# Kernel optimization log

Hardware: AMD Instinct MI355X
Metric: run time of the kernel (lower is better)

## Reference

```python
import jax, jax.numpy as jnp
import numpy as np

TEMP = 0.07
HARD_K = 512
EMB_D = 768
PROJ_D = 128
QUEUE = 32768
BATCH = 2048
NUM_CLASSES = 2


def setup_inputs() -> dict:
    key = jax.random.key(0)
    ks = jax.random.split(key, 8)
    embeddings = jax.random.normal(ks[0], (BATCH, EMB_D), dtype=jnp.float32)
    labels = jax.random.randint(ks[1], (BATCH,), 0, NUM_CLASSES)
    # projector params: Linear(D,D) -> ReLU -> Linear(D,128)
    W1 = jax.random.normal(ks[2], (EMB_D, EMB_D), dtype=jnp.float32) * 0.02
    b1 = jnp.zeros((EMB_D,), dtype=jnp.float32)
    W2 = jax.random.normal(ks[3], (EMB_D, PROJ_D), dtype=jnp.float32) * 0.02
    b2 = jnp.zeros((PROJ_D,), dtype=jnp.float32)
    # queue buffers: L2-normalized random embeddings (as in __init__) with valid labels
    qe = jax.random.normal(ks[4], (QUEUE, PROJ_D), dtype=jnp.float32)
    queue_embeddings = qe / jnp.linalg.norm(qe, axis=1, keepdims=True)
    queue_labels = jax.random.randint(ks[5], (QUEUE,), 0, NUM_CLASSES)
    return {
        'embeddings': embeddings, 'labels': labels,
        'W1': W1, 'b1': b1, 'W2': W2, 'b2': b2,
        'queue_embeddings': queue_embeddings, 'queue_labels': queue_labels,
    }


def reference(embeddings, labels, W1, b1, W2, b2, queue_embeddings, queue_labels):
    n = embeddings.shape[0]
    # projector + L2 normalize
    h = jax.nn.relu(embeddings @ W1 + b1)
    z = h @ W2 + b2
    z = z / jnp.linalg.norm(z, axis=1, keepdims=True)  # (N, 128)

    # pairwise in-batch similarities, scaled by temperature
    S = (z @ z.T) / TEMP  # (N, N)
    same = labels[:, None] == labels[None, :]
    eye = jnp.eye(n, dtype=bool)
    pos_mask = same & ~eye           # positives: same label, not self
    neg_mask = ~same                 # in-batch negatives: different label

    # logsumexp over in-batch negatives per anchor (-inf rows -> -inf, handled by logaddexp)
    neg_batch = jnp.where(neg_mask, S, -jnp.inf)
    lse_batch = jax.scipy.special.logsumexp(neg_batch, axis=1)  # (N,)

    # hard negatives from queue: opposite-label, top-K by similarity
    sims_q = z @ queue_embeddings.T  # (N, Q)
    opp = (queue_labels[None, :] != labels[:, None]) & (queue_labels[None, :] >= 0)
    masked_q = jnp.where(opp, sims_q, -jnp.inf)
    topk_vals, _ = jax.lax.top_k(masked_q, HARD_K)  # (N, K); -inf pads drop from logsumexp
    # fallback (no opposite-label entries): first K queue embeddings regardless of label
    fallback = sims_q[:, :HARD_K]
    has_opp = opp.any(axis=1, keepdims=True)
    neg_q = jnp.where(has_opp, topk_vals, fallback) / TEMP
    lse_queue = jax.scipy.special.logsumexp(neg_q, axis=1)  # (N,)

    # all negatives for anchor i: batch negatives ++ queue hard negatives
    lse_neg = jnp.logaddexp(lse_batch, lse_queue)  # (N,)

    # per positive pair (i, j): log_prob = pos_sim - logsumexp([pos_sim, negs])
    log_prob = S - jnp.logaddexp(S, lse_neg[:, None])  # (N, N)
    losses = jnp.where(pos_mask, -log_prob, 0.0)
    count = pos_mask.sum()
    return jnp.where(count > 0, losses.sum() / count.astype(losses.dtype), 0.0)
```

## Files before the change

kernel.cpp:

```cpp
#include <hip/hip_runtime.h>
#include <hip/hip_fp16.h>

#define BATCH_N   2048
#define EMB_D_    768
#define PROJ_D_   128
#define QUEUE_N   32768
#define HARD_K_   512
static constexpr float INV_T  = 1.0f / 0.07f;
static constexpr float WLO    = 0.12f;
static constexpr float S8ENC  = 255.0f / 0.88f;
static constexpr float BINW   = 0.88f / 255.0f;

typedef __attribute__((ext_vector_type(8))) short short8;
typedef __attribute__((ext_vector_type(4))) short short4v;
typedef __attribute__((ext_vector_type(4))) float f32x4;

__device__ __forceinline__ unsigned short f2bf(float f) {
    unsigned u = __float_as_uint(f);
    unsigned r = u + 0x7fffu + ((u >> 16) & 1u);
    return (unsigned short)(r >> 16);
}
__device__ __forceinline__ float bf2f(short s) {
    return __uint_as_float(((unsigned)(unsigned short)s) << 16);
}
__device__ __forceinline__ int opp_of(int mylab, const int* __restrict__ qcnt) {
    const int same = (mylab == 0) ? qcnt[0] : ((mylab == 1) ? qcnt[1] : 0);
    return qcnt[2] - same;
}

__global__ void __launch_bounds__(256) mfma_s_pack(const short* __restrict__ Ab,
                                                   const short* __restrict__ Bb,
                                                   short* __restrict__ C, int N) {
    __shared__ __align__(16) short As[128 * 128];
    __shared__ __align__(16) short Bs[128 * 128];
    const int t = threadIdx.x;
    const int lane = t & 63, wv = t >> 6;
    const int l16 = lane & 15, l4 = lane >> 4;
    const int m0 = blockIdx.y * 128, n0 = blockIdx.x * 128;

    #pragma unroll
    for (int it = 0; it < 8; ++it) {
        const int r = it * 4 + wv, row = r * 4 + l4, cg = l16 ^ (row & 15);
        __builtin_amdgcn_global_load_lds(
            (const __attribute__((address_space(1))) void*)(Ab + (size_t)(m0 + row) * 128 + cg * 8),
            (__attribute__((address_space(3))) void*)(As + r * 512), 16, 0, 0);
    }
    #pragma unroll
    for (int it = 0; it < 8; ++it) {
        const int r = it * 4 + wv, row = r * 4 + l4, cg = l16 ^ (row & 15);
        __builtin_amdgcn_global_load_lds(
            (const __attribute__((address_space(1))) void*)(Bb + (size_t)(n0 + row) * 128 + cg * 8),
            (__attribute__((address_space(3))) void*)(Bs + r * 512), 16, 0, 0);
    }
    __syncthreads();

    const int wm = (wv & 1) * 64, wn = (wv >> 1) * 64;
    f32x4 acc[4][4];
    #pragma unroll
    for (int i = 0; i < 4; ++i)
        #pragma unroll
        for (int j = 0; j < 4; ++j) acc[i][j] = f32x4{0.f, 0.f, 0.f, 0.f};

    #pragma unroll
    for (int ks = 0; ks < 4; ++ks) {
        short8 af[4], bfr[4];
        const int ch = (ks * 4 + l4) ^ l16;
        #pragma unroll
        for (int i = 0; i < 4; ++i) {
            af[i]  = *(const short8*)(As + (wm + i * 16 + l16) * 128 + ch * 8);
            bfr[i] = *(const short8*)(Bs + (wn + i * 16 + l16) * 128 + ch * 8);
        }
        #pragma unroll
        for (int i = 0; i < 4; ++i)
            #pragma unroll
            for (int j = 0; j < 4; ++j)
                acc[i][j] = __builtin_amdgcn_mfma_f32_16x16x32_bf16(af[i], bfr[j], acc[i][j], 0, 0, 0);
    }
    #pragma unroll
    for (int i = 0; i < 4; ++i)
        #pragma unroll
        for (int r = 0; r < 4; ++r) {
            const int m = m0 + wm + i * 16 + l4 * 4 + r;
            union { unsigned short u[4]; uint2 d; } pk;
            #pragma unroll
            for (int j = 0; j < 4; ++j) pk.u[j] = f2bf(acc[i][j][r]);
            *(uint2*)(C + (size_t)m * N + n0 + wn + l16 * 4) = pk.d;
        }
}

__global__ void __launch_bounds__(256) mfma_mask8(const short* __restrict__ Ab,
                                                  const short* __restrict__ Bb,
                                                  unsigned char* __restrict__ codes,
                                                  const int* __restrict__ labA,
                                                  const int* __restrict__ labB) {
    __shared__ __align__(16) short As[128 * 128];
    __shared__ __align__(16) short Bs[128 * 128];
    const int t = threadIdx.x;
    const int lane = t & 63, wv = t >> 6;
    const int l16 = lane & 15, l4 = lane >> 4;
    const int m0 = blockIdx.y * 128;
    const int wm = (wv & 1) * 64, wn = (wv >> 1) * 64;

    #pragma unroll
    for (int it = 0; it < 8; ++it) {
        const int r = it * 4 + wv, row = r * 4 + l4, cg = l16 ^ (row & 15);
        __builtin_amdgcn_global_load_lds(
            (const __attribute__((address_space(1))) void*)(Ab + (size_t)(m0 + row) * 128 + cg * 8),
            (__attribute__((address_space(3))) void*)(As + r * 512), 16, 0, 0);
    }
    {
        const int n0 = (blockIdx.x * 4) * 128;
        #pragma unroll
        for (int it = 0; it < 8; ++it) {
            const int r = it * 4 + wv, row = r * 4 + l4, cg = l16 ^ (row & 15);
            __builtin_amdgcn_global_load_lds(
                (const __attribute__((address_space(1))) void*)(Bb + (size_t)(n0 + row) * 128 + cg * 8),
                (__attribute__((address_space(3))) void*)(Bs + r * 512), 16, 0, 0);
        }
    }

    int la[16];
    #pragma unroll
    for (int i = 0; i < 4; ++i)
        #pragma unroll
        for (int r = 0; r < 4; ++r)
            la[i * 4 + r] = labA[m0 + wm + i * 16 + l4 * 4 + r];
    const float C0 = 1.0f - WLO * S8ENC;
    __syncthreads();

    #pragma unroll
    for (int tt = 0; tt < 4; ++tt) {
        const int n0 = (blockIdx.x * 4 + tt) * 128;

        f32x4 acc[4][4];
        #pragma unroll
        for (int i = 0; i < 4; ++i)
            #pragma unroll
            for (int j = 0; j < 4; ++j) acc[i][j] = f32x4{0.f, 0.f, 0.f, 0.f};

        #pragma unroll
        for (int ks = 0; ks < 4; ++ks) {
            short8 af[4], bfr[4];
            const int ch = (ks * 4 + l4) ^ l16;
            #pragma unroll
            for (int i = 0; i < 4; ++i) {
                af[i]  = *(const short8*)(As + (wm + i * 16 + l16) * 128 + ch * 8);
                bfr[i] = *(const short8*)(Bs + (wn + i * 16 + l16) * 128 + ch * 8);
            }
            #pragma unroll
            for (int i = 0; i < 4; ++i)
                #pragma unroll
                for (int j = 0; j < 4; ++j)
                    acc[i][j] = __builtin_amdgcn_mfma_f32_16x16x32_bf16(af[i], bfr[j], acc[i][j], 0, 0, 0);
        }

        if (tt < 3) {
            __syncthreads();
            const int n1 = (blockIdx.x * 4 + tt + 1) * 128;
            #pragma unroll
            for (int it = 0; it < 8; ++it) {
                const int r = it * 4 + wv, row = r * 4 + l4, cg = l16 ^ (row & 15);
                __builtin_amdgcn_global_load_lds(
                    (const __attribute__((address_space(1))) void*)(Bb + (size_t)(n1 + row) * 128 + cg * 8),
                    (__attribute__((address_space(3))) void*)(Bs + r * 512), 16, 0, 0);
            }
        }

        float a0[4], a1[4];
        #pragma unroll
        for (int j = 0; j < 4; ++j) {
            const int q = labB[n0 + wn + j * 16 + l16];
            a0[j] = (q >= 0 && q != 0) ? C0 : -1e9f;
            a1[j] = (q >= 0 && q != 1) ? C0 : -1e9f;
        }
        #pragma unroll
        for (int i = 0; i < 4; ++i) {
            #pragma unroll
            for (int r = 0; r < 4; ++r) {
                const int m  = m0 + wm + i * 16 + l4 * 4 + r;
                const bool z = (la[i * 4 + r] == 0);
                unsigned pk = 0;
                #pragma unroll
                for (int j = 0; j < 4; ++j) {
                    const float add = z ? a0[j] : a1[j];
                    const float f = fmaf(acc[i][j][r], S8ENC, add);
#if __has_builtin(__builtin_amdgcn_cvt_pk_u8_f32)
                    pk = __builtin_amdgcn_cvt_pk_u8_f32(f, j, pk);
#else
                    const unsigned c = (unsigned)fminf(fmaxf(f, 0.0f), 255.0f);
                    pk |= c << (8 * j);
#endif
                }
                *(unsigned*)(codes + (size_t)m * QUEUE_N + n0 + wn + l16 * 4) = pk;
            }
        }
        if (tt < 3) __syncthreads();
    }
}

__global__ void __launch_bounds__(256) mfma_h64(const short* __restrict__ Ab,
                                                const short* __restrict__ Bb,
                                                const float* __restrict__ bias,
                                                short* __restrict__ C,
                                                int N, int K) {
    __shared__ __align__(16) short As[64 * 128];
    __shared__ __align__(16) short Bs[128 * 128];
    const int t = threadIdx.x;
    const int lane = t & 63, wv = t >> 6;
    const int l16 = lane & 15, l4 = lane >> 4;
    const int m0 = blockIdx.y * 64, n0 = blockIdx.x * 128;
    const int wn = wv * 32;

    f32x4 acc[4][2];
    #pragma unroll
    for (int i = 0; i < 4; ++i)
        #pragma unroll
        for (int j = 0; j < 2; ++j) acc[i][j] = f32x4{0.f, 0.f, 0.f, 0.f};

    for (int kb = 0; kb < K; kb += 128) {
        __syncthreads();
        #pragma unroll
        for (int it = 0; it < 4; ++it) {
            const int r = it * 4 + wv, row = r * 4 + l4, cg = l16 ^ (row & 15);
            __builtin_amdgcn_global_load_lds(
                (const __attribute__((address_space(1))) void*)(Ab + (size_t)(m0 + row) * K + kb + cg * 8),
                (__attribute__((address_space(3))) void*)(As + r * 512), 16, 0, 0);
        }
        #pragma unroll
        for (int it = 0; it < 8; ++it) {
            const int r = it * 4 + wv, row = r * 4 + l4, cg = l16 ^ (row & 15);
            __builtin_amdgcn_global_load_lds(
                (const __attribute__((address_space(1))) void*)(Bb + (size_t)(n0 + row) * K + kb + cg * 8),
                (__attribute__((address_space(3))) void*)(Bs + r * 512), 16, 0, 0);
        }
        __syncthreads();
        #pragma unroll
        for (int ks = 0; ks < 4; ++ks) {
            short8 af[4], bfr[2];
            const int ch = (ks * 4 + l4) ^ l16;
            #pragma unroll
            for (int i = 0; i < 4; ++i)
                af[i] = *(const short8*)(As + (i * 16 + l16) * 128 + ch * 8);
            #pragma unroll
            for (int j = 0; j < 2; ++j)
                bfr[j] = *(const short8*)(Bs + (wn + j * 16 + l16) * 128 + ch * 8);
            #pragma unroll
            for (int i = 0; i < 4; ++i)
                #pragma unroll
                for (int j = 0; j < 2; ++j)
                    acc[i][j] = __builtin_amdgcn_mfma_f32_16x16x32_bf16(af[i], bfr[j], acc[i][j], 0, 0, 0);
        }
    }

    float bsv[2];
    #pragma unroll
    for (int j = 0; j < 2; ++j) bsv[j] = bias[n0 + wn + j * 16 + l16];
    #pragma unroll
    for (int i = 0; i < 4; ++i)
        #pragma unroll
        for (int r = 0; r < 4; ++r) {
            const int m = m0 + i * 16 + l4 * 4 + r;
            #pragma unroll
            for (int j = 0; j < 2; ++j) {
                const int n = n0 + wn + j * 16 + l16;
                const float v = fmaxf(acc[i][j][r] + bsv[j], 0.0f);
                C[(size_t)m * N + n] = (short)f2bf(v);
            }
        }
}

__global__ void __launch_bounds__(256) mfma_z_norm64(const short* __restrict__ Ab,
                                                     const short* __restrict__ Bb,
                                                     const float* __restrict__ bias,
                                                     short* __restrict__ zb) {
    __shared__ __align__(16) short As[64 * 128];
    __shared__ __align__(16) short Bs[128 * 128];
    __shared__ float ssq[64];
    const int t = threadIdx.x;
    const int lane = t & 63, wv = t >> 6;
    const int l16 = lane & 15, l4 = lane >> 4;
    const int m0 = blockIdx.x * 64;
    const int wn = wv * 32;
    const int K = EMB_D_;

    if (t < 64) ssq[t] = 0.0f;

    f32x4 acc[4][2];
    #pragma unroll
    for (int i = 0; i < 4; ++i)
        #pragma unroll
        for (int j = 0; j < 2; ++j) acc[i][j] = f32x4{0.f, 0.f, 0.f, 0.f};

    for (int kb = 0; kb < K; kb += 128) {
        __syncthreads();
        #pragma unroll
        for (int it = 0; it < 4; ++it) {
            const int r = it * 4 + wv, row = r * 4 + l4, cg = l16 ^ (row & 15);
            __builtin_amdgcn_global_load_lds(
                (const __attribute__((address_space(1))) void*)(Ab + (size_t)(m0 + row) * K + kb + cg * 8),
                (__attribute__((address_space(3))) void*)(As + r * 512), 16, 0, 0);
        }
        #pragma unroll
        for (int it = 0; it < 8; ++it) {
            const int r = it * 4 + wv, row = r * 4 + l4, cg = l16 ^ (row & 15);
            __builtin_amdgcn_global_load_lds(
                (const __attribute__((address_space(1))) void*)(Bb + (size_t)(row) * K + kb + cg * 8),
                (__attribute__((address_space(3))) void*)(Bs + r * 512), 16, 0, 0);
        }
        __syncthreads();
        #pragma unroll
        for (int ks = 0; ks < 4; ++ks) {
            short8 af[4], bfr[2];
            const int ch = (ks * 4 + l4) ^ l16;
            #pragma unroll
            for (int i = 0; i < 4; ++i)
                af[i] = *(const short8*)(As + (i * 16 + l16) * 128 + ch * 8);
            #pragma unroll
            for (int j = 0; j < 2; ++j)
                bfr[j] = *(const short8*)(Bs + (wn + j * 16 + l16) * 128 + ch * 8);
            #pragma unroll
            for (int i = 0; i < 4; ++i)
                #pragma unroll
                for (int j = 0; j < 2; ++j)
                    acc[i][j] = __builtin_amdgcn_mfma_f32_16x16x32_bf16(af[i], bfr[j], acc[i][j], 0, 0, 0);
        }
    }

    float bsv[2];
    #pragma unroll
    for (int j = 0; j < 2; ++j) bsv[j] = bias[wn + j * 16 + l16];
    #pragma unroll
    for (int i = 0; i < 4; ++i)
        #pragma unroll
        for (int r = 0; r < 4; ++r) {
            float p = 0.0f;
            #pragma unroll
            for (int j = 0; j < 2; ++j) {
                acc[i][j][r] += bsv[j];
                p += acc[i][j][r] * acc[i][j][r];
            }
            #pragma unroll
            for (int o = 8; o > 0; o >>= 1) p += __shfl_xor(p, o);
            if (l16 == 0) atomicAdd(&ssq[i * 16 + l4 * 4 + r], p);
        }
    __syncthreads();
    #pragma unroll
    for (int i = 0; i < 4; ++i)
        #pragma unroll
        for (int r = 0; r < 4; ++r) {
            const int lrow = i * 16 + l4 * 4 + r;
            const float inv = rsqrtf(ssq[lrow]);
            #pragma unroll
            for (int j = 0; j < 2; ++j)
                zb[(size_t)(m0 + lrow) * PROJ_D_ + wn + j * 16 + l16] =
                    (short)f2bf(acc[i][j][r] * inv);
        }
}

__global__ void __launch_bounds__(256) prep(const float* __restrict__ emb, short* __restrict__ embb,
                                            const float* __restrict__ queue, short* __restrict__ qb,
                                            const int* __restrict__ qlab, int* __restrict__ qcnt,
                                            const float* __restrict__ W1, short* __restrict__ w1t,
                                            const float* __restrict__ W2, short* __restrict__ w2t) {
    __shared__ float tile[64][65];
    const int b = blockIdx.x, t = threadIdx.x;
    if (b < 1536) {
        const int i = b * 256 + t;
        const float4 f = ((const float4*)emb)[i];
        short4v o = {(short)f2bf(f.x), (short)f2bf(f.y), (short)f2bf(f.z), (short)f2bf(f.w)};
        ((short4v*)embb)[i] = o;
    } else if (b < 5632) {
        const int i = (b - 1536) * 256 + t;
        const float4 f = ((const float4*)queue)[i];
        short4v o = {(short)f2bf(f.x), (short)f2bf(f.y), (short)f2bf(f.z), (short)f2bf(f.w)};
        ((short4v*)qb)[i] = o;
    } else if (b < 5664) {
        const int i = (b - 5632) * 256 + t;
        int c0 = 0, c1 = 0, cv = 0;
        for (int j = i; j < QUEUE_N; j += 8192) {
            const int q = qlab[j];
            c0 += (q == 0); c1 += (q == 1); cv += (q >= 0);
        }
        #pragma unroll
        for (int o = 32; o > 0; o >>= 1) {
            c0 += __shfl_xor(c0, o); c1 += __shfl_xor(c1, o); cv += __shfl_xor(cv, o);
        }
        if ((t & 63) == 0) {
            atomicAdd(&qcnt[0], c0); atomicAdd(&qcnt[1], c1); atomicAdd(&qcnt[2], cv);
        }
    } else {
        const int bid = b - 5664;
        const float* A; short* At; int R, C, bx, by;
        if (bid < 144) { A = W1; At = w1t; R = EMB_D_; C = EMB_D_;  bx = (bid % 12) * 64; by = (bid / 12) * 64; }
        else { const int b2 = bid - 144; A = W2; At = w2t; R = EMB_D_; C = PROJ_D_; bx = (b2 & 1) * 64; by = (b2 >> 1) * 64; }
        const int tc = t & 63, tg = t >> 6;
        #pragma unroll
        for (int i = 0; i < 16; i++) {
            const int r = tg * 16 + i;
            tile[r][tc] = A[(size_t)(by + r) * C + bx + tc];
        }
        __syncthreads();
        #pragma unroll
        for (int i = 0; i < 16; i++) {
            const int r = tg * 16 + i;
            At[(size_t)(bx + r) * R + by + tc] = (short)f2bf(tile[tc][r]);
        }
    }
}

__global__ void __launch_bounds__(256) topk_lse_u8(const unsigned char* __restrict__ codes,
                                                   const int* __restrict__ qcnt,
                                                   const int* __restrict__ labels,
                                                   float* __restrict__ lseq,
                                                   int* __restrict__ flag) {
    const int row = blockIdx.x, t = threadIdx.x;
    __shared__ int hist[256];
    __shared__ int suf[256];
    __shared__ int s_bin;
    __shared__ float scf[4];
    hist[t] = 0;
    __syncthreads();

    const uint4* rowp = (const uint4*)(codes + (size_t)row * QUEUE_N);
    #pragma unroll
    for (int k = 0; k < 8; k++) {
        const uint4 u = rowp[k * 256 + t];
        const unsigned w[4] = {u.x, u.y, u.z, u.w};
        #pragma unroll
        for (int q = 0; q < 4; q++)
            #pragma unroll
            for (int s = 0; s < 4; s++) {
                const int c = (w[q] >> (8 * s)) & 0xFF;
                if (c) atomicAdd(&hist[c], 1);
            }
    }
    __syncthreads();

    suf[t] = hist[t];
    __syncthreads();
    for (int off = 1; off < 256; off <<= 1) {
        int add = (t + off < 256) ? suf[t + off] : 0;
        __syncthreads();
        suf[t] += add;
        __syncthreads();
    }
    const int total = suf[1];
    const int opp   = opp_of(labels[row], qcnt);
    if (total < HARD_K_ || opp < HARD_K_) {
        if (t == 0) flag[row] = 0;
        return;
    }
    {
        const int above = (t < 255) ? suf[t + 1] : 0;
        if (suf[t] >= HARD_K_ && above < HARD_K_) s_bin = t;
    }
    __syncthreads();
    const int b = s_bin;

    float e = 0.0f;
    if (t > b && hist[t]) e = (float)hist[t] * __expf((WLO + ((float)t - 0.5f) * BINW - 1.0f) * INV_T);
    #pragma unroll
    for (int o = 32; o > 0; o >>= 1) e += __shfl_xor(e, o);
    if ((t & 63) == 0) scf[t >> 6] = e;
    __syncthreads();
    if (t == 0) {
        const float Eab  = scf[0] + scf[1] + scf[2] + scf[3];
        const int   cab  = (b < 255) ? suf[b + 1] : 0;
        const float ebin = __expf((WLO + ((float)b - 0.5f) * BINW - 1.0f) * INV_T);
        const float sadj = Eab + (float)(HARD_K_ - cab) * ebin;
        lseq[row] = INV_T + __logf(sadj);
        flag[row] = 1;
    }
}

__device__ __forceinline__ void find_crossing(int* hist, int* grp, int target,
                                              int* s_bin, int* s_chi) {
    const int t = threadIdx.x;
    const int b0 = hist[4*t], b1 = hist[4*t+1], b2 = hist[4*t+2], b3 = hist[4*t+3];
    grp[t] = b0 + b1 + b2 + b3;
    __syncthreads();
    for (int off = 1; off < 256; off <<= 1) {
        int add = (t + off < 256) ? grp[t + off] : 0;
        __syncthreads();
        grp[t] += add;
        __syncthreads();
    }
    int cab = (t < 255) ? grp[t + 1] : 0;
    const int hb[4] = {b0, b1, b2, b3};
    #pragma unroll
    for (int i = 3; i >= 0; i--) {
        const int h = hb[i];
        if (cab < target && cab + h >= target) { *s_bin = 4*t + i; *s_chi = cab; }
        cab += h;
    }
    __syncthreads();
}

#define FOR_ALL_VALS(BODY)                                                   \
    _Pragma("unroll")                                                        \
    for (int _k = 0; _k < 64; _k++) {                                        \
        const float2 _f = __half22float2(*(const __half2*)&dv[_k]);          \
        { const float v = _f.x; BODY }                                       \
        { const float v = _f.y; BODY }                                       \
    }

__global__ void __launch_bounds__(256) topk_lse_fallback(const short* __restrict__ zb,
                                                         const short* __restrict__ qb,
                                                         const int* __restrict__ labels,
                                                         const int* __restrict__ qlab,
                                                         const int* __restrict__ qcnt,
                                                         const int* __restrict__ flag,
                                                         float* __restrict__ lseq) {
    const int row = blockIdx.x, t = threadIdx.x;
    if (flag[row]) return;
    const int opp = opp_of(labels[row], qcnt);

    __shared__ float zrow[128];
    __shared__ int hist[1024];
    __shared__ int grp[256];
    __shared__ int s_bin, s_chi, s_bin2, s_chi2;
    __shared__ float scf[4]; __shared__ int sci[4];
    if (t < 128) zrow[t] = bf2f(zb[(size_t)row * 128 + t]);
    __syncthreads();

    const int mylab = labels[row];
    unsigned dv[64];
    float rm = -1e30f, rs = 0.0f;
    for (int k = 0; k < 128; k++) {
        const int j = t + 256 * k;
        float d = 0.0f;
        #pragma unroll
        for (int c = 0; c < 16; ++c) {
            const short8 qv = *(const short8*)(qb + (size_t)j * 128 + c * 8);
            #pragma unroll
            for (int e = 0; e < 8; ++e) d += zrow[c * 8 + e] * bf2f(qv[e]);
        }
        if (j < HARD_K_) {
            const float sv = d * INV_T;
            if (sv > rm) { rs = rs * __expf(rm - sv) + 1.0f; rm = sv; }
            else         { rs += __expf(sv - rm); }
        }
        const int q = qlab[j];
        const float mv = (q != mylab && q >= 0) ? d : -65504.0f;
        const __half h = __float2half(mv);
        unsigned short* p = (unsigned short*)&dv[k >> 1];
        p[k & 1] = *(const unsigned short*)&h;
    }

    if (opp == 0) {
        #pragma unroll
        for (int o = 32; o > 0; o >>= 1) {
            const float om = __shfl_xor(rm, o), os = __shfl_xor(rs, o);
            const float nm = fmaxf(rm, om);
            rs = rs * __expf(rm - nm) + os * __expf(om - nm);
            rm = nm;
        }
        if ((t & 63) == 0) { scf[t >> 6] = rm; ((float*)sci)[t >> 6] = rs; }
        __syncthreads();
        if (t == 0) {
            float M = -1e30f, Sx = 0.0f;
            for (int w = 0; w < 4; w++) {
                const float nm = fmaxf(M, scf[w]);
                Sx = Sx * __expf(M - nm) + ((float*)sci)[w] * __expf(scf[w] - nm);
                M = nm;
            }
            lseq[row] = M + __logf(Sx);
        }
        return;
    }
    if (opp < HARD_K_) {
        float mm = -1e30f, ss = 0.0f;
        FOR_ALL_VALS(
            if (v > -60000.0f) {
                const float sv = v * INV_T;
                if (sv > mm) { ss = ss * __expf(mm - sv) + 1.0f; mm = sv; }
                else         { ss += __expf(sv - mm); }
            } )
        #pragma unroll
        for (int o = 32; o > 0; o >>= 1) {
            const float om = __shfl_xor(mm, o), os = __shfl_xor(ss, o);
            const float nm = fmaxf(mm, om);
            ss = ss * __expf(mm - nm) + os * __expf(om - nm);
            mm = nm;
        }
        if ((t & 63) == 0) { scf[t >> 6] = mm; ((float*)sci)[t >> 6] = ss; }
        __syncthreads();
        if (t == 0) {
            float M = -1e30f, Sx = 0.0f;
            for (int w = 0; w < 4; w++) {
                const float nm = fmaxf(M, scf[w]);
                Sx = Sx * __expf(M - nm) + ((float*)sci)[w] * __expf(scf[w] - nm);
                M = nm;
            }
            lseq[row] = M + __logf(Sx);
        }
        return;
    }

    float mloc = -1e30f;
    FOR_ALL_VALS( mloc = fmaxf(mloc, v); )
    #pragma unroll
    for (int o = 32; o > 0; o >>= 1) mloc = fmaxf(mloc, __shfl_xor(mloc, o));
    if ((t & 63) == 0) scf[t >> 6] = mloc;
    __syncthreads();
    const float m = fmaxf(fmaxf(scf[0], scf[1]), fmaxf(scf[2], scf[3]));

    int c1 = 0, c2 = 0;
    const float w1 = m - 0.25f, w2 = m - 1.0f;
    FOR_ALL_VALS( c1 += (v >= w1); c2 += (v >= w2); )
    #pragma unroll
    for (int o = 32; o > 0; o >>= 1) { c1 += __shfl_xor(c1, o); c2 += __shfl_xor(c2, o); }
    if ((t & 63) == 0) { sci[t >> 6] = c1; }
    __syncthreads();
    const int C1 = sci[0] + sci[1] + sci[2] + sci[3];
    __syncthreads();
    if ((t & 63) == 0) { sci[t >> 6] = c2; }
    __syncthreads();
    const int C2 = sci[0] + sci[1] + sci[2] + sci[3];

    float lo;
    if      (C1 >= HARD_K_) lo = w1;
    else if (C2 >= HARD_K_) lo = w2;
    else                    lo = -1.01f;
    const float range = m - lo;
    const float scale = 1024.0f / range;

    for (int k = t; k < 1024; k += 256) hist[k] = 0;
    __syncthreads();
    FOR_ALL_VALS(
        if (v >= lo) {
            const float bf = fminf((v - lo) * scale, 1023.0f);
            atomicAdd(&hist[(int)bf], 1);
        } )
    __syncthreads();
    find_crossing(hist, grp, HARD_K_, &s_bin, &s_chi);
    const int   bin1 = s_bin, chi1 = s_chi;
    const float binw = range * (1.0f / 1024.0f);
    const float lo1  = lo + bin1 * binw;
    const float ssc  = 1024.0f / binw;

    for (int k = t; k < 1024; k += 256) hist[k] = 0;
    __syncthreads();
    FOR_ALL_VALS(
        if (v >= lo) {
            const float bf = fminf((v - lo) * scale, 1023.0f);
            if ((int)bf == bin1) {
                const float sf = fminf(fmaxf((v - lo1) * ssc, 0.0f), 1023.0f);
                atomicAdd(&hist[(int)sf], 1);
            }
        } )
    __syncthreads();
    find_crossing(hist, grp, HARD_K_ - chi1, &s_bin2, &s_chi2);
    const float thr = lo1 + s_bin2 * (binw * (1.0f / 1024.0f));

    float sl = 0.0f; int cg = 0;
    FOR_ALL_VALS( if (v > thr) { cg++; sl += __expf((v - m) * INV_T); } )
    #pragma unroll
    for (int o = 32; o > 0; o >>= 1) { sl += __shfl_xor(sl, o); cg += __shfl_xor(cg, o); }
    if ((t & 63) == 0) { scf[t >> 6] = sl; sci[t >> 6] = cg; }
    __syncthreads();
    if (t == 0) {
        const float slt = scf[0] + scf[1] + scf[2] + scf[3];
        const int   cgt = sci[0] + sci[1] + sci[2] + sci[3];
        const float sadj = slt + ((float)HARD_K_ - (float)cgt) * __expf((thr - m) * INV_T);
        lseq[row] = m * INV_T + __logf(sadj);
    }
}

__global__ void __launch_bounds__(256) batch_row_loss(const short* __restrict__ S,
                                                      const int* __restrict__ labels,
                                                      const float* __restrict__ lse_queue,
                                                      float* __restrict__ part_out,
                                                      int* __restrict__ cnt_out) {
    const int t = threadIdx.x;
    const int wv = t >> 6, lane = t & 63;
    const int row = blockIdx.x * 4 + wv;
    __shared__ int plab[BATCH_N];
    for (int idx = t; idx < BATCH_N; idx += 256) {
        const int col = (idx & ~63) + ((idx & 3) << 4) + ((idx >> 2) & 15);
        plab[idx] = labels[col];
    }
    __syncthreads();
    const int myLab = labels[row];
    const uint4* rp = (const uint4*)(S + (size_t)row * BATCH_N);

    float v[32]; int lb[32];
    #pragma unroll
    for (int kk = 0; kk < 4; kk++) {
        const uint4 u = rp[lane + 64 * kk];
        const unsigned w[4] = {u.x, u.y, u.z, u.w};
        const int base = (lane + 64 * kk) * 8;
        #pragma unroll
        for (int q = 0; q < 4; q++) {
            v[kk * 8 + 2 * q]     = __uint_as_float(w[q] << 16);
            v[kk * 8 + 2 * q + 1] = __uint_as_float(w[q] & 0xFFFF0000u);
            lb[kk * 8 + 2 * q]     = plab[base + 2 * q];
            lb[kk * 8 + 2 * q + 1] = plab[base + 2 * q + 1];
        }
    }

    const float REF = INV_T;
    float sneg = 0.0f;
    #pragma unroll
    for (int k = 0; k < 32; k++) {
        const float ev = __expf(v[k] * INV_T - REF);
        sneg += (lb[k] != myLab) ? ev : 0.0f;
    }
    #pragma unroll
    for (int o = 32; o > 0; o >>= 1) sneg += __shfl_xor(sneg, o);
    const float lseb = (sneg > 0.0f) ? REF + __logf(sneg) : -1e30f;
    const float Lq = lse_queue[row];
    const float mx0 = fmaxf(lseb, Lq), mn0 = fminf(lseb, Lq);
    const float L = mx0 + __logf(1.0f + __expf(mn0 - mx0));

    float part = 0.0f; int cnt = 0;
    #pragma unroll
    for (int k = 0; k < 32; k++) {
        const int idx = ((lane + 64 * (k >> 3)) * 8) + (k & 7);
        const int col = (idx & ~63) + ((idx & 3) << 4) + ((idx >> 2) & 15);
        if (lb[k] == myLab && col != row) {
            const float sv = v[k] * INV_T;
            const float mx = fmaxf(sv, L), mn = fminf(sv, L);
            part += (mx - sv) + __logf(1.0f + __expf(mn - mx));
            cnt++;
        }
    }
    #pragma unroll
    for (int o = 32; o > 0; o >>= 1) { part += __shfl_xor(part, o); cnt += __shfl_xor(cnt, o); }
    if (lane == 0) { part_out[row] = part; cnt_out[row] = cnt; }
}

__global__ void __launch_bounds__(256) finalize_loss(const float* __restrict__ part,
                                                     const int* __restrict__ cnt,
                                                     float* __restrict__ out) {
    const int t = threadIdx.x;
    float s = 0.0f; int c = 0;
    #pragma unroll
    for (int k = 0; k < 8; k++) { s += part[t + 256 * k]; c += cnt[t + 256 * k]; }
    #pragma unroll
    for (int o = 32; o > 0; o >>= 1) { s += __shfl_xor(s, o); c += __shfl_xor(c, o); }
    __shared__ float sf[4]; __shared__ int sc[4];
    if ((t & 63) == 0) { sf[t >> 6] = s; sc[t >> 6] = c; }
    __syncthreads();
    if (t == 0) {
        const float st = sf[0] + sf[1] + sf[2] + sf[3];
        const int   ct = sc[0] + sc[1] + sc[2] + sc[3];
        out[0] = (ct > 0) ? (st / (float)ct) : 0.0f;
    }
}

extern "C" void kernel_launch(void* const* d_in, const int* in_sizes, int n_in,
                              void* d_out, int out_size, void* d_ws, size_t ws_size,
                              hipStream_t stream) {
    const float* emb    = (const float*)d_in[0];
    const int*   labels = (const int*)  d_in[1];
    const float* W1     = (const float*)d_in[2];
    const float* b1     = (const float*)d_in[3];
    const float* W2     = (const float*)d_in[4];
    const float* b2     = (const float*)d_in[5];
    const float* queue  = (const float*)d_in[6];
    const int*   qlab   = (const int*)  d_in[7];

    char* ws = (char*)d_ws;
    short*         Sbuf  = (short*)        (ws);
    unsigned char* codes = (unsigned char*)(ws + 16777216);
    short*         embb  = (short*)        (ws + 83886080);
    short*         hbf   = (short*)        (ws + 87031808);
    short*         zb    = (short*)        (ws + 90177536);
    short*         qb    = (short*)        (ws + 90701824);
    short*         w1t   = (short*)        (ws + 99090432);
    short*         w2t   = (short*)        (ws + 100270080);
    float*         lseq  = (float*)        (ws + 100466688);
    int*           flag  = (int*)          (ws + 100474880);
    int*           qcnt  = (int*)          (ws + 100483072);
    float*         partb = (float*)        (ws + 100483136);
    int*           cntb  = (int*)          (ws + 100491328);

    hipMemsetAsync(ws + 100474880, 0, 8192 + 64, stream);

    dim3 blk(256);
    prep<<<dim3(5832), blk, 0, stream>>>(emb, embb, queue, qb, qlab, qcnt, W1, w1t, W2, w2t);
    mfma_h64<<<dim3(EMB_D_ / 128, BATCH_N / 64), blk, 0, stream>>>(embb, w1t, b1, hbf, EMB_D_, EMB_D_);
    mfma_z_norm64<<<dim3(BATCH_N / 64), blk, 0, stream>>>(hbf, w2t, b2, zb);
    mfma_mask8<<<dim3(QUEUE_N / 512, BATCH_N / 128), blk, 0, stream>>>(zb, qb, codes, labels, qlab);
    topk_lse_u8<<<BATCH_N, blk, 0, stream>>>(codes, qcnt, labels, lseq, flag);
    topk_lse_fallback<<<BATCH_N, blk, 0, stream>>>(zb, qb, labels, qlab, qcnt, flag, lseq);
    mfma_s_pack<<<dim3(BATCH_N / 128, BATCH_N / 128), blk, 0, stream>>>(zb, zb, Sbuf, BATCH_N);
    batch_row_loss<<<BATCH_N / 4, blk, 0, stream>>>(Sbuf, labels, lseq, partb, cntb);
    finalize_loss<<<1, blk, 0, stream>>>(partb, cntb, (float*)d_out);
}
```

Baseline: 168.6 us.

## Build per-row similarity histograms with global atomics instead of a u8 code matrix

The masked queue-similarity GEMM no longer writes a full 2048x32768 byte code matrix. Each nonzero code now increments a per-row 256-bin histogram in global memory with atomics, and the top-k kernel just reads that 256-entry row histogram. The histogram buffer is zeroed by extra blocks in the prep kernel. This removes roughly 64MB of writes and 64MB of reads, in exchange for millions of scattered global atomics whose contention cost depends on how sparse the above-threshold codes are.

```diff
diff --git a/kernel.cpp b/kernel.cpp
--- a/kernel.cpp
+++ b/kernel.cpp
@@ -90,7 +90,7 @@
 
 __global__ void __launch_bounds__(256) mfma_mask8(const short* __restrict__ Ab,
                                                   const short* __restrict__ Bb,
-                                                  unsigned char* __restrict__ codes,
+                                                  int* __restrict__ ghist,
                                                   const int* __restrict__ labA,
                                                   const int* __restrict__ labB) {
     __shared__ __align__(16) short As[128 * 128];
@@ -191,7 +191,14 @@
                     pk |= c << (8 * j);
 #endif
                 }
-                *(unsigned*)(codes + (size_t)m * QUEUE_N + n0 + wn + l16 * 4) = pk;
+                if (pk) {
+                    int* hrow = ghist + (size_t)m * 256;
+                    #pragma unroll
+                    for (int j = 0; j < 4; ++j) {
+                        const unsigned c = (pk >> (8 * j)) & 0xFFu;
+                        if (c) atomicAdd(hrow + c, 1);
+                    }
+                }
             }
         }
         if (tt < 3) __syncthreads();
@@ -361,7 +368,8 @@
                                             const float* __restrict__ queue, short* __restrict__ qb,
                                             const int* __restrict__ qlab, int* __restrict__ qcnt,
                                             const float* __restrict__ W1, short* __restrict__ w1t,
-                                            const float* __restrict__ W2, short* __restrict__ w2t) {
+                                            const float* __restrict__ W2, short* __restrict__ w2t,
+                                            int* __restrict__ ghist) {
     __shared__ float tile[64][65];
     const int b = blockIdx.x, t = threadIdx.x;
     if (b < 1536) {
@@ -388,7 +396,7 @@
         if ((t & 63) == 0) {
             atomicAdd(&qcnt[0], c0); atomicAdd(&qcnt[1], c1); atomicAdd(&qcnt[2], cv);
         }
-    } else {
+    } else if (b < 5832) {
         const int bid = b - 5664;
         const float* A; short* At; int R, C, bx, by;
         if (bid < 144) { A = W1; At = w1t; R = EMB_D_; C = EMB_D_;  bx = (bid % 12) * 64; by = (bid / 12) * 64; }
@@ -405,38 +413,24 @@
             const int r = tg * 16 + i;
             At[(size_t)(bx + r) * R + by + tc] = (short)f2bf(tile[tc][r]);
         }
-    }
-}
-
-__global__ void __launch_bounds__(256) topk_lse_u8(const unsigned char* __restrict__ codes,
-                                                   const int* __restrict__ qcnt,
-                                                   const int* __restrict__ labels,
-                                                   float* __restrict__ lseq,
-                                                   int* __restrict__ flag) {
+    } else {
+        const uint4 zz = {0u, 0u, 0u, 0u};
+        ((uint4*)ghist)[(size_t)(b - 5832) * 256 + t] = zz;
+    }
+}
+
+__global__ void __launch_bounds__(256) topk_lse_hist(const int* __restrict__ ghist,
+                                                     const int* __restrict__ qcnt,
+                                                     const int* __restrict__ labels,
+                                                     float* __restrict__ lseq,
+                                                     int* __restrict__ flag) {
     const int row = blockIdx.x, t = threadIdx.x;
-    __shared__ int hist[256];
     __shared__ int suf[256];
     __shared__ int s_bin;
     __shared__ float scf[4];
-    hist[t] = 0;
-    __syncthreads();
-
-    const uint4* rowp = (const uint4*)(codes + (size_t)row * QUEUE_N);
-    #pragma unroll
-    for (int k = 0; k < 8; k++) {
-        const uint4 u = rowp[k * 256 + t];
-        const unsigned w[4] = {u.x, u.y, u.z, u.w};
-        #pragma unroll
-        for (int q = 0; q < 4; q++)
-            #pragma unroll
-            for (int s = 0; s < 4; s++) {
-                const int c = (w[q] >> (8 * s)) & 0xFF;
-                if (c) atomicAdd(&hist[c], 1);
-            }
-    }
-    __syncthreads();
-
-    suf[t] = hist[t];
+
+    const int h = ghist[(size_t)row * 256 + t];
+    suf[t] = h;
     __syncthreads();
     for (int off = 1; off < 256; off <<= 1) {
         int add = (t + off < 256) ? suf[t + off] : 0;
@@ -458,7 +452,7 @@
     const int b = s_bin;
 
     float e = 0.0f;
-    if (t > b && hist[t]) e = (float)hist[t] * __expf((WLO + ((float)t - 0.5f) * BINW - 1.0f) * INV_T);
+    if (t > b && h) e = (float)h * __expf((WLO + ((float)t - 0.5f) * BINW - 1.0f) * INV_T);
     #pragma unroll
     for (int o = 32; o > 0; o >>= 1) e += __shfl_xor(e, o);
     if ((t & 63) == 0) scf[t >> 6] = e;
@@ -763,7 +757,7 @@
 
     char* ws = (char*)d_ws;
     short*         Sbuf  = (short*)        (ws);
-    unsigned char* codes = (unsigned char*)(ws + 16777216);
+    int*           ghist = (int*)          (ws + 16777216);
     short*         embb  = (short*)        (ws + 83886080);
     short*         hbf   = (short*)        (ws + 87031808);
     short*         zb    = (short*)        (ws + 90177536);
@@ -779,11 +773,11 @@
     hipMemsetAsync(ws + 100474880, 0, 8192 + 64, stream);
 
     dim3 blk(256);
-    prep<<<dim3(5832), blk, 0, stream>>>(emb, embb, queue, qb, qlab, qcnt, W1, w1t, W2, w2t);
+    prep<<<dim3(6344), blk, 0, stream>>>(emb, embb, queue, qb, qlab, qcnt, W1, w1t, W2, w2t, ghist);
     mfma_h64<<<dim3(EMB_D_ / 128, BATCH_N / 64), blk, 0, stream>>>(embb, w1t, b1, hbf, EMB_D_, EMB_D_);
     mfma_z_norm64<<<dim3(BATCH_N / 64), blk, 0, stream>>>(hbf, w2t, b2, zb);
-    mfma_mask8<<<dim3(QUEUE_N / 512, BATCH_N / 128), blk, 0, stream>>>(zb, qb, codes, labels, qlab);
-    topk_lse_u8<<<BATCH_N, blk, 0, stream>>>(codes, qcnt, labels, lseq, flag);
+    mfma_mask8<<<dim3(QUEUE_N / 512, BATCH_N / 128), blk, 0, stream>>>(zb, qb, ghist, labels, qlab);
+    topk_lse_hist<<<BATCH_N, blk, 0, stream>>>(ghist, qcnt, labels, lseq, flag);
     topk_lse_fallback<<<BATCH_N, blk, 0, stream>>>(zb, qb, labels, qlab, qcnt, flag, lseq);
     mfma_s_pack<<<dim3(BATCH_N / 128, BATCH_N / 128), blk, 0, stream>>>(zb, zb, Sbuf, BATCH_N);
     batch_row_loss<<<BATCH_N / 4, blk, 0, stream>>>(Sbuf, labels, lseq, partb, cntb);
```

New measurement: 257.4 us. 52.7% more time.

## Sort queue and batch rows by label to skip same-label similarity tiles

Applied to the files above, without the earlier changes.

Adds a permutation kernel that groups queue columns and batch rows by label. The masked similarity GEMM then skips 512-column tiles holding only same-label entries, and the top-k histogram kernel scans only the opposite-label column range of each permuted row. This cuts roughly half the GEMM work, code writes and histogram reads, at the cost of an extra kernel launch, gathered loads through index arrays, and atomic-based ordering.

```diff
diff --git a/kernel.cpp b/kernel.cpp
--- a/kernel.cpp
+++ b/kernel.cpp
@@ -91,30 +91,44 @@
 __global__ void __launch_bounds__(256) mfma_mask8(const short* __restrict__ Ab,
                                                   const short* __restrict__ Bb,
                                                   unsigned char* __restrict__ codes,
-                                                  const int* __restrict__ labA,
-                                                  const int* __restrict__ labB) {
+                                                  const int* __restrict__ rlabp,
+                                                  const int* __restrict__ qlabp,
+                                                  const int* __restrict__ colidx,
+                                                  const int* __restrict__ rowmap,
+                                                  const int* __restrict__ qcnt,
+                                                  const int* __restrict__ rcnt) {
+    const int m0 = blockIdx.y * 128;
+    const int c0 = qcnt[0], c1v = qcnt[1], r0 = rcnt[0];
+    int lo, hi;
+    if (m0 + 128 <= r0)      { lo = c0; hi = c0 + c1v; }
+    else if (m0 >= r0)       { lo = 0;  hi = c0; }
+    else                     { lo = 0;  hi = c0 + c1v; }
+    const int bs = blockIdx.x * 512;
+    if (bs + 512 <= lo || bs >= hi) return;
+
     __shared__ __align__(16) short As[128 * 128];
     __shared__ __align__(16) short Bs[128 * 128];
     const int t = threadIdx.x;
     const int lane = t & 63, wv = t >> 6;
     const int l16 = lane & 15, l4 = lane >> 4;
-    const int m0 = blockIdx.y * 128;
     const int wm = (wv & 1) * 64, wn = (wv >> 1) * 64;
 
     #pragma unroll
     for (int it = 0; it < 8; ++it) {
         const int r = it * 4 + wv, row = r * 4 + l4, cg = l16 ^ (row & 15);
+        const int srow = rowmap[m0 + row];
         __builtin_amdgcn_global_load_lds(
-            (const __attribute__((address_space(1))) void*)(Ab + (size_t)(m0 + row) * 128 + cg * 8),
+            (const __attribute__((address_space(1))) void*)(Ab + (size_t)srow * 128 + cg * 8),
             (__attribute__((address_space(3))) void*)(As + r * 512), 16, 0, 0);
     }
     {
-        const int n0 = (blockIdx.x * 4) * 128;
+        const int n0 = bs;
         #pragma unroll
         for (int it = 0; it < 8; ++it) {
             const int r = it * 4 + wv, row = r * 4 + l4, cg = l16 ^ (row & 15);
+            const int scol = colidx[n0 + row];
             __builtin_amdgcn_global_load_lds(
-                (const __attribute__((address_space(1))) void*)(Bb + (size_t)(n0 + row) * 128 + cg * 8),
+                (const __attribute__((address_space(1))) void*)(Bb + (size_t)scol * 128 + cg * 8),
                 (__attribute__((address_space(3))) void*)(Bs + r * 512), 16, 0, 0);
         }
     }
@@ -124,13 +138,13 @@
     for (int i = 0; i < 4; ++i)
         #pragma unroll
         for (int r = 0; r < 4; ++r)
-            la[i * 4 + r] = labA[m0 + wm + i * 16 + l4 * 4 + r];
+            la[i * 4 + r] = rlabp[m0 + wm + i * 16 + l4 * 4 + r];
     const float C0 = 1.0f - WLO * S8ENC;
     __syncthreads();
 
     #pragma unroll
     for (int tt = 0; tt < 4; ++tt) {
-        const int n0 = (blockIdx.x * 4 + tt) * 128;
+        const int n0 = bs + tt * 128;
 
         f32x4 acc[4][4];
         #pragma unroll
@@ -156,12 +170,13 @@
 
         if (tt < 3) {
             __syncthreads();
-            const int n1 = (blockIdx.x * 4 + tt + 1) * 128;
+            const int n1 = bs + (tt + 1) * 128;
             #pragma unroll
             for (int it = 0; it < 8; ++it) {
                 const int r = it * 4 + wv, row = r * 4 + l4, cg = l16 ^ (row & 15);
+                const int scol = colidx[n1 + row];
                 __builtin_amdgcn_global_load_lds(
-                    (const __attribute__((address_space(1))) void*)(Bb + (size_t)(n1 + row) * 128 + cg * 8),
+                    (const __attribute__((address_space(1))) void*)(Bb + (size_t)scol * 128 + cg * 8),
                     (__attribute__((address_space(3))) void*)(Bs + r * 512), 16, 0, 0);
             }
         }
@@ -169,7 +184,7 @@
         float a0[4], a1[4];
         #pragma unroll
         for (int j = 0; j < 4; ++j) {
-            const int q = labB[n0 + wn + j * 16 + l16];
+            const int q = qlabp[n0 + wn + j * 16 + l16];
             a0[j] = (q >= 0 && q != 0) ? C0 : -1e9f;
             a1[j] = (q >= 0 && q != 1) ? C0 : -1e9f;
         }
@@ -361,7 +376,8 @@
                                             const float* __restrict__ queue, short* __restrict__ qb,
                                             const int* __restrict__ qlab, int* __restrict__ qcnt,
                                             const float* __restrict__ W1, short* __restrict__ w1t,
-                                            const float* __restrict__ W2, short* __restrict__ w2t) {
+                                            const float* __restrict__ W2, short* __restrict__ w2t,
+                                            const int* __restrict__ labels, int* __restrict__ rcnt) {
     __shared__ float tile[64][65];
     const int b = blockIdx.x, t = threadIdx.x;
     if (b < 1536) {
@@ -388,7 +404,7 @@
         if ((t & 63) == 0) {
             atomicAdd(&qcnt[0], c0); atomicAdd(&qcnt[1], c1); atomicAdd(&qcnt[2], cv);
         }
-    } else {
+    } else if (b < 5832) {
         const int bid = b - 5664;
         const float* A; short* At; int R, C, bx, by;
         if (bid < 144) { A = W1; At = w1t; R = EMB_D_; C = EMB_D_;  bx = (bid % 12) * 64; by = (bid / 12) * 64; }
@@ -405,15 +421,89 @@
             const int r = tg * 16 + i;
             At[(size_t)(bx + r) * R + by + tc] = (short)f2bf(tile[tc][r]);
         }
+    } else {
+        int c = 0;
+        for (int j = t; j < BATCH_N; j += 256) c += (labels[j] == 0);
+        #pragma unroll
+        for (int o = 32; o > 0; o >>= 1) c += __shfl_xor(c, o);
+        if ((t & 63) == 0) atomicAdd(&rcnt[0], c);
+    }
+}
+
+__global__ void __launch_bounds__(256) build_perm(const int* __restrict__ qlab,
+                                                  const int* __restrict__ labels,
+                                                  const int* __restrict__ qcnt,
+                                                  const int* __restrict__ rcnt,
+                                                  int* __restrict__ colidx,
+                                                  int* __restrict__ qlabp,
+                                                  int* __restrict__ rowmap,
+                                                  int* __restrict__ rlabp,
+                                                  int* __restrict__ pc) {
+    const int t = threadIdx.x, lane = t & 63, wv = t >> 6;
+    __shared__ int wcnt[4][3];
+    __shared__ int gbase[3];
+    const unsigned long long below = (1ull << lane) - 1ull;
+    if (blockIdx.x < 128) {
+        const int j = blockIdx.x * 256 + t;
+        const int q = qlab[j];
+        const int cls = (q == 0) ? 0 : ((q == 1) ? 1 : 2);
+        const unsigned long long b0 = __ballot(cls == 0);
+        const unsigned long long b1 = __ballot(cls == 1);
+        const unsigned long long b2 = __ballot(cls == 2);
+        const int rank = (cls == 0) ? __popcll(b0 & below)
+                       : ((cls == 1) ? __popcll(b1 & below) : __popcll(b2 & below));
+        if (lane == 0) {
+            wcnt[wv][0] = __popcll(b0); wcnt[wv][1] = __popcll(b1); wcnt[wv][2] = __popcll(b2);
+        }
+        __syncthreads();
+        if (t < 3) {
+            const int tot = wcnt[0][t] + wcnt[1][t] + wcnt[2][t] + wcnt[3][t];
+            gbase[t] = atomicAdd(&pc[t], tot);
+        }
+        __syncthreads();
+        int wb = 0;
+        #pragma unroll
+        for (int w = 0; w < 4; ++w) if (w < wv) wb += wcnt[w][cls];
+        const int cbase = (cls == 0) ? 0 : ((cls == 1) ? qcnt[0] : qcnt[0] + qcnt[1]);
+        const int pos = cbase + gbase[cls] + wb + rank;
+        colidx[pos] = j; qlabp[pos] = q;
+    } else {
+        const int r = (blockIdx.x - 128) * 256 + t;
+        const int l = labels[r];
+        const int cls = (l == 0) ? 0 : 1;
+        const unsigned long long b0 = __ballot(cls == 0);
+        const unsigned long long b1 = __ballot(cls == 1);
+        const int rank = (cls == 0) ? __popcll(b0 & below) : __popcll(b1 & below);
+        if (lane == 0) { wcnt[wv][0] = __popcll(b0); wcnt[wv][1] = __popcll(b1); }
+        __syncthreads();
+        if (t < 2) {
+            const int tot = wcnt[0][t] + wcnt[1][t] + wcnt[2][t] + wcnt[3][t];
+            gbase[t] = atomicAdd(&pc[3 + t], tot);
+        }
+        __syncthreads();
+        int wb = 0;
+        #pragma unroll
+        for (int w = 0; w < 4; ++w) if (w < wv) wb += wcnt[w][cls];
+        const int cbase = (cls == 0) ? 0 : rcnt[0];
+        const int pos = cbase + gbase[cls] + wb + rank;
+        rowmap[pos] = r; rlabp[pos] = l;
     }
 }
 
 __global__ void __launch_bounds__(256) topk_lse_u8(const unsigned char* __restrict__ codes,
                                                    const int* __restrict__ qcnt,
-                                                   const int* __restrict__ labels,
+                                                   const int* __restrict__ rlabp,
+                                                   const int* __restrict__ rowmap,
                                                    float* __restrict__ lseq,
                                                    int* __restrict__ flag) {
-    const int row = blockIdx.x, t = threadIdx.x;
+    const int p = blockIdx.x, t = threadIdx.x;
+    const int orig  = rowmap[p];
+    const int myLab = rlabp[p];
+    const int opp   = opp_of(myLab, qcnt);
+    if (opp < HARD_K_) {
+        if (t == 0) flag[orig] = 0;
+        return;
+    }
     __shared__ int hist[256];
     __shared__ int suf[256];
     __shared__ int s_bin;
@@ -421,10 +511,15 @@
     hist[t] = 0;
     __syncthreads();
 
-    const uint4* rowp = (const uint4*)(codes + (size_t)row * QUEUE_N);
-    #pragma unroll
-    for (int k = 0; k < 8; k++) {
-        const uint4 u = rowp[k * 256 + t];
+    const int c0 = qcnt[0];
+    const int lo = (myLab == 0) ? c0 : 0;
+    const int hi = (myLab == 0) ? c0 + qcnt[1] : c0;
+    const int klo = (lo & ~511) >> 4;
+    const int khi = ((hi + 511) & ~511) >> 4;
+
+    const uint4* rowp = (const uint4*)(codes + (size_t)p * QUEUE_N);
+    for (int k = klo + t; k < khi; k += 256) {
+        const uint4 u = rowp[k];
         const unsigned w[4] = {u.x, u.y, u.z, u.w};
         #pragma unroll
         for (int q = 0; q < 4; q++)
@@ -445,9 +540,8 @@
         __syncthreads();
     }
     const int total = suf[1];
-    const int opp   = opp_of(labels[row], qcnt);
-    if (total < HARD_K_ || opp < HARD_K_) {
-        if (t == 0) flag[row] = 0;
+    if (total < HARD_K_) {
+        if (t == 0) flag[orig] = 0;
         return;
     }
     {
@@ -468,8 +562,8 @@
         const int   cab  = (b < 255) ? suf[b + 1] : 0;
         const float ebin = __expf((WLO + ((float)b - 0.5f) * BINW - 1.0f) * INV_T);
         const float sadj = Eab + (float)(HARD_K_ - cab) * ebin;
-        lseq[row] = INV_T + __logf(sadj);
-        flag[row] = 1;
+        lseq[orig] = INV_T + __logf(sadj);
+        flag[orig] = 1;
     }
 }
 
@@ -775,15 +869,22 @@
     int*           qcnt  = (int*)          (ws + 100483072);
     float*         partb = (float*)        (ws + 100483136);
     int*           cntb  = (int*)          (ws + 100491328);
-
-    hipMemsetAsync(ws + 100474880, 0, 8192 + 64, stream);
+    int*           rcnt  = (int*)          (ws + 100499520);
+    int*           pc    = (int*)          (ws + 100499584);
+    int*           colidx= (int*)          (ws + 100499648);
+    int*           qlabp = (int*)          (ws + 100630720);
+    int*           rowmap= (int*)          (ws + 100761792);
+    int*           rlabp = (int*)          (ws + 100769984);
+
+    hipMemsetAsync(ws + 100474880, 0, 24768, stream);
 
     dim3 blk(256);
-    prep<<<dim3(5832), blk, 0, stream>>>(emb, embb, queue, qb, qlab, qcnt, W1, w1t, W2, w2t);
+    prep<<<dim3(5833), blk, 0, stream>>>(emb, embb, queue, qb, qlab, qcnt, W1, w1t, W2, w2t, labels, rcnt);
+    build_perm<<<dim3(136), blk, 0, stream>>>(qlab, labels, qcnt, rcnt, colidx, qlabp, rowmap, rlabp, pc);
     mfma_h64<<<dim3(EMB_D_ / 128, BATCH_N / 64), blk, 0, stream>>>(embb, w1t, b1, hbf, EMB_D_, EMB_D_);
     mfma_z_norm64<<<dim3(BATCH_N / 64), blk, 0, stream>>>(hbf, w2t, b2, zb);
-    mfma_mask8<<<dim3(QUEUE_N / 512, BATCH_N / 128), blk, 0, stream>>>(zb, qb, codes, labels, qlab);
-    topk_lse_u8<<<BATCH_N, blk, 0, stream>>>(codes, qcnt, labels, lseq, flag);
+    mfma_mask8<<<dim3(QUEUE_N / 512, BATCH_N / 128), blk, 0, stream>>>(zb, qb, codes, rlabp, qlabp, colidx, rowmap, qcnt, rcnt);
+    topk_lse_u8<<<BATCH_N, blk, 0, stream>>>(codes, qcnt, rlabp, rowmap, lseq, flag);
     topk_lse_fallback<<<BATCH_N, blk, 0, stream>>>(zb, qb, labels, qlab, qcnt, flag, lseq);
     mfma_s_pack<<<dim3(BATCH_N / 128, BATCH_N / 128), blk, 0, stream>>>(zb, zb, Sbuf, BATCH_N);
     batch_row_loss<<<BATCH_N / 4, blk, 0, stream>>>(Sbuf, labels, lseq, partb, cntb);
```

Measured after the change: 166.4 us. Within noise of the previous version (-1.3%).
